# Performance work log

Hardware: AMD Instinct MI355X
Metric: run time of the kernel (lower is better)

The kernel has to match this reference:

```python
import jax, jax.numpy as jnp
import numpy as np

NUM_MODELS = 64
OUT_F = 256
IN_F = 256
B = 32768
F0 = 2
F1 = 2


def setup_inputs() -> dict:
    key = jax.random.key(0)
    k1, k2, k3, k4 = jax.random.split(key, 4)
    sqrt_k = float(np.sqrt(1.0 / NUM_MODELS))
    weights = 2 * sqrt_k * jax.random.uniform(k1, (NUM_MODELS, OUT_F, IN_F), dtype=jnp.float32) - sqrt_k
    biases = 2 * sqrt_k * jax.random.uniform(k2, (NUM_MODELS, OUT_F), dtype=jnp.float32) - sqrt_k
    inputs = jax.random.normal(k3, (B, IN_F // F1), dtype=jnp.float32)
    indices = jax.random.randint(k4, (B,), 0, NUM_MODELS, dtype=jnp.int64)
    return {"inputs": inputs, "weights": weights, "biases": biases,
            "indices": indices, "factor0": F0, "factor1": F1}


def reference(inputs, weights, biases, indices, factor0, factor1):
    out_sub = weights.shape[1] // factor0
    in_sub = weights.shape[2] // factor1
    # Gather per-sample weight slices: (B, out_sub, in_sub)
    subweight = weights[indices, :out_sub, :in_sub]
    subbias = biases[indices, :out_sub]  # (B, out_sub)
    # Batched matvec + bias
    return jnp.einsum('boi,bi->bo', subweight, inputs) + subbias
```

## Files before the change

kernel.cpp:

```cpp
#include <hip/hip_runtime.h>
#include <hip/hip_bf16.h>

#define NMODELS 64
#define NB      32768
#define INF     256
#define OUTF    256
#define INS     128
#define OUTS    128
#define TILE_M  64
#define LDSW    136
#define NT      16

using bf16x8  = __attribute__((ext_vector_type(8))) short;
using f32x4   = __attribute__((ext_vector_type(4))) float;
using short4v = __attribute__((ext_vector_type(4))) short;
using float4v = __attribute__((ext_vector_type(4))) float;

__device__ __forceinline__ unsigned short f2bf(float f) {
    union { float fv; unsigned u; } v; v.fv = f;
    unsigned u = v.u;
    u += 0x7fffu + ((u >> 16) & 1u);
    return (unsigned short)(u >> 16);
}

__global__ __launch_bounds__(256) void k_hist(const int* __restrict__ idx,
                                              int* __restrict__ counts) {
    __shared__ int h[NMODELS];
    const int t = threadIdx.x;
    if (t < NMODELS) h[t] = 0;
    __syncthreads();
    const int i = blockIdx.x * 256 + t;
    if (i < NB) atomicAdd(&h[idx[i]], 1);
    __syncthreads();
    if (t < NMODELS && h[t] != 0) atomicAdd(&counts[t], h[t]);
}

__global__ void k_scan(const int* __restrict__ counts,
                       int* __restrict__ starts, int* __restrict__ cursors) {
    const int lane = threadIdx.x;
    const int c = counts[lane];
    int x = c;
    #pragma unroll
    for (int d = 1; d < 64; d <<= 1) {
        int y = __shfl_up(x, d, 64);
        if (lane >= d) x += y;
    }
    const int ex = x - c;
    starts[lane]  = ex;
    cursors[lane] = ex;
}

__global__ __launch_bounds__(256) void k_scatter(const int* __restrict__ idx,
                                                 int* __restrict__ cursors,
                                                 int* __restrict__ perm) {
    __shared__ int h[NMODELS];
    __shared__ int base[NMODELS];
    const int t = threadIdx.x;
    if (t < NMODELS) h[t] = 0;
    __syncthreads();
    const int i = blockIdx.x * 256 + t;
    int m = -1, r = 0;
    if (i < NB) { m = idx[i]; r = atomicAdd(&h[m], 1); }
    __syncthreads();
    if (t < NMODELS && h[t] != 0) base[t] = atomicAdd(&cursors[t], h[t]);
    __syncthreads();
    if (m >= 0) perm[base[m] + r] = i;
}

__global__ __launch_bounds__(256) void k_gemm(const float* __restrict__ x,
                                              const float* __restrict__ w,
                                              const float* __restrict__ bias,
                                              const int* __restrict__ starts,
                                              const int* __restrict__ counts,
                                              const int* __restrict__ perm,
                                              float* __restrict__ out) {
    __shared__ __align__(16) unsigned short Ws[OUTS * LDSW];
    __shared__ __align__(16) unsigned short Xs[TILE_M * LDSW];
    __shared__ float bias_s[OUTS];
    __shared__ int rowid[TILE_M];

    const int m   = blockIdx.x;
    const int cnt = counts[m];
    if ((int)blockIdx.y * TILE_M >= cnt) return;
    const int start = starts[m];
    const int t = threadIdx.x;

    const float* wm = w + (size_t)m * (OUTF * INF);
    #pragma unroll
    for (int c = 0; c < 16; ++c) {
        const int e   = c * 256 + t;
        const int row = e >> 5;
        const int c4  = e & 31;
        float4v v = *(const float4v*)(wm + row * INF + c4 * 4);
        short4v s;
        s.x = (short)f2bf(v.x); s.y = (short)f2bf(v.y);
        s.z = (short)f2bf(v.z); s.w = (short)f2bf(v.w);
        *(short4v*)&Ws[row * LDSW + c4 * 4] = s;
    }
    if (t < OUTS) bias_s[t] = bias[m * OUTF + t];

    const int wave = t >> 6;
    const int lane = t & 63;
    const int quad = lane >> 4;
    const int lr   = lane & 15;

    for (int tile = blockIdx.y; tile * TILE_M < cnt; tile += NT) {
        const int row0 = tile * TILE_M;
        const int rows = min(TILE_M, cnt - row0);
        __syncthreads();

        #pragma unroll
        for (int c = 0; c < 8; ++c) {
            const int e   = c * 256 + t;
            const int row = e >> 5;
            const int c4  = e & 31;
            short4v s;
            if (row < rows) {
                const int g = perm[start + row0 + row];
                if (c4 == 0) rowid[row] = g;
                float4v v = *(const float4v*)(x + (size_t)g * INS + c4 * 4);
                s.x = (short)f2bf(v.x); s.y = (short)f2bf(v.y);
                s.z = (short)f2bf(v.z); s.w = (short)f2bf(v.w);
            } else {
                s = (short4v){0, 0, 0, 0};
                if (c4 == 0) rowid[row] = -1;
            }
            *(short4v*)&Xs[row * LDSW + c4 * 4] = s;
        }
        __syncthreads();

        f32x4 acc[8];
        #pragma unroll
        for (int nt = 0; nt < 8; ++nt) acc[nt] = (f32x4){0.f, 0.f, 0.f, 0.f};

        const int arow = wave * 16 + lr;
        #pragma unroll
        for (int k0 = 0; k0 < INS; k0 += 32) {
            bf16x8 a = *(const bf16x8*)&Xs[arow * LDSW + k0 + quad * 8];
            #pragma unroll
            for (int nt = 0; nt < 8; ++nt) {
                bf16x8 b = *(const bf16x8*)&Ws[(nt * 16 + lr) * LDSW + k0 + quad * 8];
                acc[nt] = __builtin_amdgcn_mfma_f32_16x16x32_bf16(a, b, acc[nt], 0, 0, 0);
            }
        }

        #pragma unroll
        for (int nt = 0; nt < 8; ++nt) {
            const int o  = nt * 16 + lr;
            const float bv = bias_s[o];
            #pragma unroll
            for (int r = 0; r < 4; ++r) {
                const int srow = wave * 16 + quad * 4 + r;
                const int g = rowid[srow];
                if (g >= 0) out[(size_t)g * OUTS + o] = acc[nt][r] + bv;
            }
        }
    }
}

extern "C" void kernel_launch(void* const* d_in, const int* in_sizes, int n_in,
                              void* d_out, int out_size, void* d_ws, size_t ws_size,
                              hipStream_t stream) {
    const float* x    = (const float*)d_in[0];
    const float* w    = (const float*)d_in[1];
    const float* bias = (const float*)d_in[2];
    const int*   idx  = (const int*)d_in[3];
    float* out = (float*)d_out;

    int* ws      = (int*)d_ws;
    int* counts  = ws;
    int* starts  = ws + 64;
    int* cursors = ws + 128;
    int* perm    = ws + 192;

    hipMemsetAsync(counts, 0, 64 * sizeof(int), stream);
    k_hist   <<<dim3(NB / 256), dim3(256), 0, stream>>>(idx, counts);
    k_scan   <<<dim3(1),        dim3(64),  0, stream>>>(counts, starts, cursors);
    k_scatter<<<dim3(NB / 256), dim3(256), 0, stream>>>(idx, cursors, perm);
    k_gemm   <<<dim3(NMODELS, NT), dim3(256), 0, stream>>>(x, w, bias, starts, counts, perm, out);
}
```

Before: 104.1 us.

## Restructure pipeline: fused prep kernel, deterministic scatter, async LDS weight loads, register A-fragments

The pipeline drops from five launches to three. Weight bf16 conversion is moved into a prep kernel that also builds per-block histograms. The scatter kernel computes prefix offsets from the partial histograms, which removes the memset, the scan kernel and the global atomics. The GEMM loads pre-swizzled bf16 weights into LDS with async global_load_lds, converts X straight into register A-fragments with no X LDS staging or per-tile barriers, and writes whole output rows. NT drops from 16 to 10. The cost is an extra bf16 weight buffer in workspace and a full weight-conversion pass each call.

```diff
diff --git a/kernel.cpp b/kernel.cpp
--- a/kernel.cpp
+++ b/kernel.cpp
@@ -8,151 +8,178 @@
 #define INS     128
 #define OUTS    128
 #define TILE_M  64
-#define LDSW    136
-#define NT      16
-
+#define NT      10
+#define NHB     128
+#define WCONV_BLOCKS 512
+
+typedef unsigned int u32;
+typedef unsigned short u16;
 using bf16x8  = __attribute__((ext_vector_type(8))) short;
 using f32x4   = __attribute__((ext_vector_type(4))) float;
-using short4v = __attribute__((ext_vector_type(4))) short;
 using float4v = __attribute__((ext_vector_type(4))) float;
-
-__device__ __forceinline__ unsigned short f2bf(float f) {
-    union { float fv; unsigned u; } v; v.fv = f;
-    unsigned u = v.u;
+using short8v = __attribute__((ext_vector_type(8))) short;
+
+__device__ __forceinline__ u16 f2bf(float f) {
+    union { float fv; u32 u; } v; v.fv = f;
+    u32 u = v.u;
     u += 0x7fffu + ((u >> 16) & 1u);
-    return (unsigned short)(u >> 16);
-}
-
-__global__ __launch_bounds__(256) void k_hist(const int* __restrict__ idx,
-                                              int* __restrict__ counts) {
-    __shared__ int h[NMODELS];
+    return (u16)(u >> 16);
+}
+
+__device__ __forceinline__ void async_copy16(const void* g, void* l) {
+    __builtin_amdgcn_global_load_lds((const __attribute__((address_space(1))) u32*)g,
+                                     (__attribute__((address_space(3))) u32*)l,
+                                     16, 0, 0);
+}
+
+__global__ __launch_bounds__(256) void k_prep(const int* __restrict__ idx,
+                                              const float* __restrict__ w,
+                                              int* __restrict__ hist_part,
+                                              u16* __restrict__ wb) {
     const int t = threadIdx.x;
-    if (t < NMODELS) h[t] = 0;
+    const int b = blockIdx.x;
+    if (b < WCONV_BLOCKS) {
+        const int cid = b * 256 + t;
+        const int m   = cid >> 11;
+        const int rem = cid & 2047;
+        const int row = rem >> 4;
+        const int c   = rem & 15;
+        const float* src = w + ((size_t)m * OUTF + row) * INF + c * 8;
+        float4v v0 = *(const float4v*)(src);
+        float4v v1 = *(const float4v*)(src + 4);
+        short8v s;
+        s[0]=(short)f2bf(v0.x); s[1]=(short)f2bf(v0.y); s[2]=(short)f2bf(v0.z); s[3]=(short)f2bf(v0.w);
+        s[4]=(short)f2bf(v1.x); s[5]=(short)f2bf(v1.y); s[6]=(short)f2bf(v1.z); s[7]=(short)f2bf(v1.w);
+        *(short8v*)(wb + ((size_t)(m * 128 + row) * 128) + ((c ^ (row & 15)) * 8)) = s;
+    } else {
+        __shared__ int h[NMODELS];
+        const int b2 = b - WCONV_BLOCKS;
+        if (t < NMODELS) h[t] = 0;
+        __syncthreads();
+        atomicAdd(&h[idx[b2 * 256 + t]], 1);
+        __syncthreads();
+        if (t < NMODELS) hist_part[b2 * NMODELS + t] = h[t];
+    }
+}
+
+__global__ __launch_bounds__(256) void k_scatter(const int* __restrict__ idx,
+                                                 const int* __restrict__ hist_part,
+                                                 int* __restrict__ starts_g,
+                                                 int* __restrict__ counts_g,
+                                                 int* __restrict__ perm) {
+    __shared__ int H[NHB * NMODELS];
+    __shared__ int starts_s[NMODELS];
+    __shared__ int pre_s[NMODELS];
+    __shared__ int lh[NMODELS];
+    const int t = threadIdx.x;
+    const int b = blockIdx.x;
+    #pragma unroll
+    for (int k = 0; k < (NHB * NMODELS) / 256; ++k)
+        H[k * 256 + t] = hist_part[k * 256 + t];
+    if (t < NMODELS) lh[t] = 0;
     __syncthreads();
-    const int i = blockIdx.x * 256 + t;
-    if (i < NB) atomicAdd(&h[idx[i]], 1);
+    if (t < NMODELS) {
+        int sum = 0, pre = 0;
+        for (int bb = 0; bb < NHB; ++bb) {
+            if (bb == b) pre = sum;
+            sum += H[bb * NMODELS + t];
+        }
+        pre_s[t] = pre;
+        int x = sum;
+        #pragma unroll
+        for (int d = 1; d < 64; d <<= 1) {
+            int y = __shfl_up(x, d, 64);
+            if (t >= d) x += y;
+        }
+        starts_s[t] = x - sum;
+        if (b == 0) { starts_g[t] = x - sum; counts_g[t] = sum; }
+    }
     __syncthreads();
-    if (t < NMODELS && h[t] != 0) atomicAdd(&counts[t], h[t]);
-}
-
-__global__ void k_scan(const int* __restrict__ counts,
-                       int* __restrict__ starts, int* __restrict__ cursors) {
-    const int lane = threadIdx.x;
-    const int c = counts[lane];
-    int x = c;
-    #pragma unroll
-    for (int d = 1; d < 64; d <<= 1) {
-        int y = __shfl_up(x, d, 64);
-        if (lane >= d) x += y;
-    }
-    const int ex = x - c;
-    starts[lane]  = ex;
-    cursors[lane] = ex;
-}
-
-__global__ __launch_bounds__(256) void k_scatter(const int* __restrict__ idx,
-                                                 int* __restrict__ cursors,
-                                                 int* __restrict__ perm) {
-    __shared__ int h[NMODELS];
-    __shared__ int base[NMODELS];
-    const int t = threadIdx.x;
-    if (t < NMODELS) h[t] = 0;
-    __syncthreads();
-    const int i = blockIdx.x * 256 + t;
-    int m = -1, r = 0;
-    if (i < NB) { m = idx[i]; r = atomicAdd(&h[m], 1); }
-    __syncthreads();
-    if (t < NMODELS && h[t] != 0) base[t] = atomicAdd(&cursors[t], h[t]);
-    __syncthreads();
-    if (m >= 0) perm[base[m] + r] = i;
+    const int i = b * 256 + t;
+    const int m = idx[i];
+    const int r = atomicAdd(&lh[m], 1);
+    perm[starts_s[m] + pre_s[m] + r] = i;
 }
 
 __global__ __launch_bounds__(256) void k_gemm(const float* __restrict__ x,
-                                              const float* __restrict__ w,
+                                              const u16* __restrict__ wb,
                                               const float* __restrict__ bias,
-                                              const int* __restrict__ starts,
-                                              const int* __restrict__ counts,
+                                              const int* __restrict__ starts_g,
+                                              const int* __restrict__ counts_g,
                                               const int* __restrict__ perm,
                                               float* __restrict__ out) {
-    __shared__ __align__(16) unsigned short Ws[OUTS * LDSW];
-    __shared__ __align__(16) unsigned short Xs[TILE_M * LDSW];
-    __shared__ float bias_s[OUTS];
-    __shared__ int rowid[TILE_M];
-
+    __shared__ __align__(16) u16 Ws[OUTS * 128];
     const int m   = blockIdx.x;
-    const int cnt = counts[m];
+    const int cnt = counts_g[m];
     if ((int)blockIdx.y * TILE_M >= cnt) return;
-    const int start = starts[m];
-    const int t = threadIdx.x;
-
-    const float* wm = w + (size_t)m * (OUTF * INF);
-    #pragma unroll
-    for (int c = 0; c < 16; ++c) {
-        const int e   = c * 256 + t;
-        const int row = e >> 5;
-        const int c4  = e & 31;
-        float4v v = *(const float4v*)(wm + row * INF + c4 * 4);
-        short4v s;
-        s.x = (short)f2bf(v.x); s.y = (short)f2bf(v.y);
-        s.z = (short)f2bf(v.z); s.w = (short)f2bf(v.w);
-        *(short4v*)&Ws[row * LDSW + c4 * 4] = s;
-    }
-    if (t < OUTS) bias_s[t] = bias[m * OUTF + t];
-
+    const int start = starts_g[m];
+    const int t    = threadIdx.x;
     const int wave = t >> 6;
     const int lane = t & 63;
     const int quad = lane >> 4;
     const int lr   = lane & 15;
 
+    {
+        const char* g = (const char*)(wb + (size_t)m * (OUTS * 128));
+        char* l = (char*)Ws;
+        #pragma unroll
+        for (int itc = 0; itc < 8; ++itc) {
+            const int off = itc * 4096 + wave * 1024;
+            async_copy16(g + off + lane * 16, l + off);
+        }
+    }
+    float bv[8];
+    #pragma unroll
+    for (int nt = 0; nt < 8; ++nt) bv[nt] = bias[m * OUTF + nt * 16 + lr];
+
+    int xoff[4];
+    #pragma unroll
+    for (int k0 = 0; k0 < 4; ++k0) xoff[k0] = ((k0 * 4 + quad) ^ lr) * 8;
+    const int rowbase = lr * 128;
+
+    __syncthreads();
+
     for (int tile = blockIdx.y; tile * TILE_M < cnt; tile += NT) {
-        const int row0 = tile * TILE_M;
-        const int rows = min(TILE_M, cnt - row0);
-        __syncthreads();
-
-        #pragma unroll
-        for (int c = 0; c < 8; ++c) {
-            const int e   = c * 256 + t;
-            const int row = e >> 5;
-            const int c4  = e & 31;
-            short4v s;
-            if (row < rows) {
-                const int g = perm[start + row0 + row];
-                if (c4 == 0) rowid[row] = g;
-                float4v v = *(const float4v*)(x + (size_t)g * INS + c4 * 4);
-                s.x = (short)f2bf(v.x); s.y = (short)f2bf(v.y);
-                s.z = (short)f2bf(v.z); s.w = (short)f2bf(v.w);
-            } else {
-                s = (short4v){0, 0, 0, 0};
-                if (c4 == 0) rowid[row] = -1;
-            }
-            *(short4v*)&Xs[row * LDSW + c4 * 4] = s;
-        }
-        __syncthreads();
-
+        const int row0 = tile * TILE_M + wave * 16;
+        int p = -1;
+        if (row0 + lr < cnt) p = perm[start + row0 + lr];
+        const int gx = (p >= 0) ? p : 0;
+        const float* xr = x + (size_t)gx * INS + quad * 8;
+        f32x4 xa[8];
+        #pragma unroll
+        for (int k0 = 0; k0 < 4; ++k0) {
+            xa[2 * k0]     = *(const float4v*)(xr + k0 * 32);
+            xa[2 * k0 + 1] = *(const float4v*)(xr + k0 * 32 + 4);
+        }
+        bf16x8 afr[4];
+        #pragma unroll
+        for (int k0 = 0; k0 < 4; ++k0) {
+            bf16x8 a;
+            a[0] = (short)f2bf(xa[2*k0].x); a[1] = (short)f2bf(xa[2*k0].y);
+            a[2] = (short)f2bf(xa[2*k0].z); a[3] = (short)f2bf(xa[2*k0].w);
+            a[4] = (short)f2bf(xa[2*k0+1].x); a[5] = (short)f2bf(xa[2*k0+1].y);
+            a[6] = (short)f2bf(xa[2*k0+1].z); a[7] = (short)f2bf(xa[2*k0+1].w);
+            afr[k0] = a;
+        }
         f32x4 acc[8];
         #pragma unroll
         for (int nt = 0; nt < 8; ++nt) acc[nt] = (f32x4){0.f, 0.f, 0.f, 0.f};
-
-        const int arow = wave * 16 + lr;
-        #pragma unroll
-        for (int k0 = 0; k0 < INS; k0 += 32) {
-            bf16x8 a = *(const bf16x8*)&Xs[arow * LDSW + k0 + quad * 8];
+        #pragma unroll
+        for (int k0 = 0; k0 < 4; ++k0) {
             #pragma unroll
             for (int nt = 0; nt < 8; ++nt) {
-                bf16x8 b = *(const bf16x8*)&Ws[(nt * 16 + lr) * LDSW + k0 + quad * 8];
-                acc[nt] = __builtin_amdgcn_mfma_f32_16x16x32_bf16(a, b, acc[nt], 0, 0, 0);
+                bf16x8 bfr = *(const bf16x8*)&Ws[nt * 2048 + rowbase + xoff[k0]];
+                acc[nt] = __builtin_amdgcn_mfma_f32_16x16x32_bf16(afr[k0], bfr, acc[nt], 0, 0, 0);
             }
         }
-
-        #pragma unroll
-        for (int nt = 0; nt < 8; ++nt) {
-            const int o  = nt * 16 + lr;
-            const float bv = bias_s[o];
-            #pragma unroll
-            for (int r = 0; r < 4; ++r) {
-                const int srow = wave * 16 + quad * 4 + r;
-                const int g = rowid[srow];
-                if (g >= 0) out[(size_t)g * OUTS + o] = acc[nt][r] + bv;
+        #pragma unroll
+        for (int r = 0; r < 4; ++r) {
+            const int g = __shfl(p, quad * 4 + r, 64);
+            if (g >= 0) {
+                float* orow = out + (size_t)g * OUTS;
+                #pragma unroll
+                for (int nt = 0; nt < 8; ++nt)
+                    orow[nt * 16 + lr] = acc[nt][r] + bv[nt];
             }
         }
     }
@@ -167,15 +194,14 @@
     const int*   idx  = (const int*)d_in[3];
     float* out = (float*)d_out;
 
-    int* ws      = (int*)d_ws;
-    int* counts  = ws;
-    int* starts  = ws + 64;
-    int* cursors = ws + 128;
-    int* perm    = ws + 192;
-
-    hipMemsetAsync(counts, 0, 64 * sizeof(int), stream);
-    k_hist   <<<dim3(NB / 256), dim3(256), 0, stream>>>(idx, counts);
-    k_scan   <<<dim3(1),        dim3(64),  0, stream>>>(counts, starts, cursors);
-    k_scatter<<<dim3(NB / 256), dim3(256), 0, stream>>>(idx, cursors, perm);
-    k_gemm   <<<dim3(NMODELS, NT), dim3(256), 0, stream>>>(x, w, bias, starts, counts, perm, out);
-}
+    int* ws        = (int*)d_ws;
+    int* hist_part = ws;
+    int* starts_g  = ws + 8192;
+    int* counts_g  = ws + 8256;
+    int* perm      = ws + 8320;
+    u16* wb        = (u16*)(ws + 8320 + 32768);
+
+    k_prep   <<<dim3(WCONV_BLOCKS + NHB), dim3(256), 0, stream>>>(idx, w, hist_part, wb);
+    k_scatter<<<dim3(NHB),                dim3(256), 0, stream>>>(idx, hist_part, starts_g, counts_g, perm);
+    k_gemm   <<<dim3(NMODELS, NT),        dim3(256), 0, stream>>>(x, wb, bias, starts_g, counts_g, perm, out);
+}
```

Result: faster. 96.05 us (-7.8%).
